# Performance work log

Measured on AMD Instinct MI355X. Metric: run time of the kernel, lower is better.

## Reference

```python
import jax, jax.numpy as jnp
import numpy as np

Q, N, C, H, W = 200, 25, 640, 5, 5
TEMPERATURE = 0.1
EPS = 1e-8  # torch F.cosine_similarity eps


def setup_inputs() -> dict:
    key = jax.random.key(0)
    k1, k2 = jax.random.split(key)
    feature_q = jax.random.normal(k1, (Q, N, C, H, W), dtype=jnp.float32)
    feature_s = jax.random.normal(k2, (Q, N, C, H, W), dtype=jnp.float32)
    return {"feature_q": feature_q, "feature_s": feature_s}


def reference(feature_q, feature_s):
    # Correlation volume: contract over channels c -> [Q, N, Hs, Ws, Hq, Wq]
    corr = jnp.einsum('qncij,qnckl->qnijkl', feature_s, feature_q)

    # Co-attention: mean-pool over the opposite spatial dims, softmax over last axis
    s_att = jax.nn.softmax(corr.mean(axis=(4, 5)), axis=-1)  # [Q, N, Hs, Ws]
    q_att = jax.nn.softmax(corr.mean(axis=(2, 3)), axis=-1)  # [Q, N, Hq, Wq]

    # Support aggregation (mode='support'):
    # torch broadcast [1,Q,N,1,H,W]*[1,Q,N,C,H,W] then mean(dim=1)
    # == mean over q of s_att[q,n,h,w] * feature_s[q,n,c,h,w] -> [1,N,C,H,W]
    attended_s = (s_att[:, :, None, :, :] * feature_s).mean(axis=0, keepdims=True)

    # Query aggregation (mode='query'):
    # torch broadcast [1,Q',N,1,H,W]*[Q,1,N,C,H,W] then mean(dim=1=Q')
    # == feature_q[q,n,c,h,w] * mean_{q'} q_att[q',n,h,w] -> [Q,N,C,H,W]
    # (fused form: avoids materializing the [Q,Q,N,C,H,W] intermediate)
    attended_q = feature_q * q_att.mean(axis=0)[None, :, None, :, :]

    # Cosine similarity along last dim (W), torch semantics with eps clamp
    dot = jnp.sum(attended_s * attended_q, axis=-1)               # [Q,N,C,H]
    norm_s = jnp.maximum(jnp.sqrt(jnp.sum(attended_s * attended_s, axis=-1)), EPS)
    norm_q = jnp.maximum(jnp.sqrt(jnp.sum(attended_q * attended_q, axis=-1)), EPS)
    similarity_score = dot / (norm_s * norm_q) / TEMPERATURE      # [Q,N,C,H]
    return similarity_score
```

## Files before the change

### kernel.cpp

```cpp
#include <hip/hip_runtime.h>

constexpr int Qn = 200;
constexpr int Nn = 25;
constexpr int Cn = 640;
constexpr int Hn = 5;
constexpr int Wn = 5;
constexpr int HWn = Hn * Wn;
constexpr int CHW = Cn * HWn;
constexpr float TEMP_INV = 10.0f;
constexpr float EPSC = 1e-8f;

typedef const float __attribute__((address_space(1)))* gbl_f;
typedef float __attribute__((address_space(3)))* lds_f;

__device__ __forceinline__ float wave_sum(float v) {
    v += __shfl_down(v, 32); v += __shfl_down(v, 16); v += __shfl_down(v, 8);
    v += __shfl_down(v, 4);  v += __shfl_down(v, 2);  v += __shfl_down(v, 1);
    return v;
}

__global__ __launch_bounds__(256) void attn_kernel(
    const float* __restrict__ fq, const float* __restrict__ fs,
    float* __restrict__ s_att, float* __restrict__ qbar)
{
    __shared__ float lds[4 * 3200];

    const int qn   = blockIdx.x;
    const int n    = qn % Nn;
    const int tid  = threadIdx.x;
    const int lane = tid & 63;
    const int wave = tid >> 6;

    const float* fq_t = fq + (size_t)qn * CHW;
    const float* fs_t = fs + (size_t)qn * CHW;
    float* ldsq = &lds[wave * 3200];
    float* ldss = ldsq + 1600;

    float ms[HWn], mq[HWn];
#pragma unroll
    for (int p = 0; p < HWn; ++p) { ms[p] = 0.f; mq[p] = 0.f; }

    for (int tile = wave; tile < 10; tile += 4) {
        const float* gq = fq_t + tile * 1600;
        const float* gs = fs_t + tile * 1600;

        asm volatile("s_waitcnt lgkmcnt(0)" ::: "memory");

#pragma unroll
        for (int i = 0; i < 6; ++i) {
            __builtin_amdgcn_global_load_lds((gbl_f)(gq + (i * 64 + lane) * 4),
                                             (lds_f)(ldsq + i * 256), 16, 0, 0);
            __builtin_amdgcn_global_load_lds((gbl_f)(gs + (i * 64 + lane) * 4),
                                             (lds_f)(ldss + i * 256), 16, 0, 0);
        }
        __builtin_amdgcn_global_load_lds((gbl_f)(gq + 1536 + lane),
                                         (lds_f)(ldsq + 1536), 4, 0, 0);
        __builtin_amdgcn_global_load_lds((gbl_f)(gs + 1536 + lane),
                                         (lds_f)(ldss + 1536), 4, 0, 0);
        asm volatile("s_waitcnt vmcnt(0)" ::: "memory");

        const float* rq = ldsq + lane * HWn;
        const float* rs = ldss + lane * HWn;
        float vq[HWn], vs[HWn];
        float sq = 0.f, ssv = 0.f;
#pragma unroll
        for (int p = 0; p < HWn; ++p) { vq[p] = rq[p]; sq += vq[p]; }
#pragma unroll
        for (int p = 0; p < HWn; ++p) { vs[p] = rs[p]; ssv += vs[p]; }
#pragma unroll
        for (int p = 0; p < HWn; ++p) {
            ms[p] += vs[p] * sq;
            mq[p] += vq[p] * ssv;
        }
    }

    __syncthreads();

    float* red = lds;
    float* fm  = lds + 200;
#pragma unroll
    for (int p = 0; p < HWn; ++p) {
        float v = wave_sum(ms[p]);
        if (lane == 0) red[wave * 50 + p] = v;
        float u = wave_sum(mq[p]);
        if (lane == 0) red[wave * 50 + HWn + p] = u;
    }
    __syncthreads();
    if (tid < 50) {
        fm[tid] = red[tid] + red[50 + tid] + red[100 + tid] + red[150 + tid];
    }
    __syncthreads();

    if (tid < 10) {
        const int r = tid;
        const float* row = (r < 5) ? &fm[r * 5] : &fm[HWn + (r - 5) * 5];
        float v[5];
        float mx = -1e30f;
#pragma unroll
        for (int j = 0; j < 5; ++j) {
            v[j] = row[j] * (1.0f / HWn);
            mx = fmaxf(mx, v[j]);
        }
        float s = 0.f;
#pragma unroll
        for (int j = 0; j < 5; ++j) { v[j] = __expf(v[j] - mx); s += v[j]; }
        const float inv = 1.0f / s;
        if (r < 5) {
#pragma unroll
            for (int j = 0; j < 5; ++j)
                s_att[(size_t)qn * HWn + r * 5 + j] = v[j] * inv;
        } else {
#pragma unroll
            for (int j = 0; j < 5; ++j)
                atomicAdd(&qbar[n * HWn + (r - 5) * 5 + j],
                          v[j] * inv * (1.0f / Qn));
        }
    }
}

__global__ __launch_bounds__(256) void agg_kernel(
    const float* __restrict__ fs, const float* __restrict__ s_att,
    float* __restrict__ att_s)
{
    constexpr int QCH = 40;
    __shared__ float w_lds[QCH * HWn];
    const int n  = blockIdx.y;
    const int q0 = blockIdx.z * QCH;

    for (int i = threadIdx.x; i < QCH * HWn; i += 256) {
        const int q = q0 + i / HWn;
        const int hw = i % HWn;
        w_lds[i] = s_att[(size_t)(q * Nn + n) * HWn + hw];
    }
    __syncthreads();

    const int f4 = blockIdx.x * 256 + threadIdx.x;
    if (f4 >= CHW / 4) return;
    const int f = f4 * 4;
    const int hw0 = f % HWn, hw1 = (f + 1) % HWn,
              hw2 = (f + 2) % HWn, hw3 = (f + 3) % HWn;

    float4 acc = make_float4(0.f, 0.f, 0.f, 0.f);
#pragma unroll 4
    for (int qi = 0; qi < QCH; ++qi) {
        const int q = q0 + qi;
        const float4 v = *(const float4*)(fs + (size_t)(q * Nn + n) * CHW + f);
        const float* w = &w_lds[qi * HWn];
        acc.x += w[hw0] * v.x;
        acc.y += w[hw1] * v.y;
        acc.z += w[hw2] * v.z;
        acc.w += w[hw3] * v.w;
    }
    float* dst = att_s + (size_t)n * CHW + f;
    atomicAdd(dst + 0, acc.x * (1.0f / Qn));
    atomicAdd(dst + 1, acc.y * (1.0f / Qn));
    atomicAdd(dst + 2, acc.z * (1.0f / Qn));
    atomicAdd(dst + 3, acc.w * (1.0f / Qn));
}

__global__ __launch_bounds__(256) void cos_kernel(
    const float* __restrict__ fq, const float* __restrict__ att_s,
    const float* __restrict__ qbar, float* __restrict__ out)
{
    const size_t idx = (size_t)blockIdx.x * 256 + threadIdx.x;
    if (idx >= (size_t)Qn * Nn * Cn * Hn) return;
    const int h = (int)(idx % Hn);
    const size_t t = idx / Hn;
    const int c = (int)(t % Cn);
    const size_t qn = t / Cn;
    const int n = (int)(qn % Nn);

    const float* fqr = fq + (qn * Cn + c) * HWn + h * Wn;
    const float* asr = att_s + ((size_t)n * Cn + c) * HWn + h * Wn;
    const float* qb  = qbar + n * HWn + h * Wn;

    float dot = 0.f, ns2 = 0.f, nq2 = 0.f;
#pragma unroll
    for (int w = 0; w < Wn; ++w) {
        const float aq = fqr[w] * qb[w];
        const float as = asr[w];
        dot += as * aq;
        ns2 += as * as;
        nq2 += aq * aq;
    }
    const float ns = fmaxf(sqrtf(ns2), EPSC);
    const float nq = fmaxf(sqrtf(nq2), EPSC);
    out[idx] = dot / (ns * nq) * TEMP_INV;
}

extern "C" void kernel_launch(void* const* d_in, const int* in_sizes, int n_in,
                              void* d_out, int out_size, void* d_ws, size_t ws_size,
                              hipStream_t stream)
{
    const float* fq = (const float*)d_in[0];
    const float* fs = (const float*)d_in[1];
    float* out = (float*)d_out;

    float* s_att = (float*)d_ws;
    float* qbar  = s_att + (size_t)Qn * Nn * HWn;
    float* att_s = qbar + 1024;

    hipMemsetAsync(qbar, 0, (1024 + (size_t)Nn * CHW) * sizeof(float), stream);

    attn_kernel<<<Qn * Nn, 256, 0, stream>>>(fq, fs, s_att, qbar);

    dim3 g2((CHW / 4 + 255) / 256, Nn, 5);
    agg_kernel<<<g2, 256, 0, stream>>>(fs, s_att, att_s);

    const size_t total = (size_t)Qn * Nn * Cn * Hn;
    cos_kernel<<<(unsigned)((total + 255) / 256), 256, 0, stream>>>(fq, att_s, qbar, out);
}
```

Baseline: 766.0 us.

## Use single-wave attention blocks with software-pipelined LDS staging

```diff
diff --git a/kernel.cpp b/kernel.cpp
--- a/kernel.cpp
+++ b/kernel.cpp
@@ -13,108 +13,111 @@
 typedef const float __attribute__((address_space(1)))* gbl_f;
 typedef float __attribute__((address_space(3)))* lds_f;
 
-__device__ __forceinline__ float wave_sum(float v) {
-    v += __shfl_down(v, 32); v += __shfl_down(v, 16); v += __shfl_down(v, 8);
-    v += __shfl_down(v, 4);  v += __shfl_down(v, 2);  v += __shfl_down(v, 1);
-    return v;
-}
-
-__global__ __launch_bounds__(256) void attn_kernel(
+__device__ __forceinline__ void stage_tile(const float* g, float* b, int lane) {
+#pragma unroll
+    for (int i = 0; i < 6; ++i)
+        __builtin_amdgcn_global_load_lds((gbl_f)(g + i * 256 + lane * 4),
+                                         (lds_f)(b + i * 256), 16, 0, 0);
+    __builtin_amdgcn_global_load_lds((gbl_f)(g + 1536 + lane),
+                                     (lds_f)(b + 1536), 4, 0, 0);
+}
+
+__global__ __launch_bounds__(64) void attn_kernel(
     const float* __restrict__ fq, const float* __restrict__ fs,
     float* __restrict__ s_att, float* __restrict__ qbar)
 {
-    __shared__ float lds[4 * 3200];
+    __shared__ float bq[1600];
+    __shared__ float bs[1600];
 
     const int qn   = blockIdx.x;
     const int n    = qn % Nn;
-    const int tid  = threadIdx.x;
-    const int lane = tid & 63;
-    const int wave = tid >> 6;
+    const int lane = threadIdx.x;
 
     const float* fq_t = fq + (size_t)qn * CHW;
     const float* fs_t = fs + (size_t)qn * CHW;
-    float* ldsq = &lds[wave * 3200];
-    float* ldss = ldsq + 1600;
+
+    stage_tile(fq_t, bq, lane);
+    stage_tile(fs_t, bs, lane);
 
     float ms[HWn], mq[HWn];
 #pragma unroll
     for (int p = 0; p < HWn; ++p) { ms[p] = 0.f; mq[p] = 0.f; }
 
-    for (int tile = wave; tile < 10; tile += 4) {
-        const float* gq = fq_t + tile * 1600;
-        const float* gs = fs_t + tile * 1600;
-
+    for (int t = 0; t < 10; ++t) {
+        asm volatile("s_waitcnt vmcnt(7)" ::: "memory");
+        float vq[HWn];
+        float sq = 0.f;
+        const float* rq = bq + lane * HWn;
+#pragma unroll
+        for (int p = 0; p < HWn; ++p) { vq[p] = rq[p]; sq += vq[p]; }
         asm volatile("s_waitcnt lgkmcnt(0)" ::: "memory");
-
-#pragma unroll
-        for (int i = 0; i < 6; ++i) {
-            __builtin_amdgcn_global_load_lds((gbl_f)(gq + (i * 64 + lane) * 4),
-                                             (lds_f)(ldsq + i * 256), 16, 0, 0);
-            __builtin_amdgcn_global_load_lds((gbl_f)(gs + (i * 64 + lane) * 4),
-                                             (lds_f)(ldss + i * 256), 16, 0, 0);
-        }
-        __builtin_amdgcn_global_load_lds((gbl_f)(gq + 1536 + lane),
-                                         (lds_f)(ldsq + 1536), 4, 0, 0);
-        __builtin_amdgcn_global_load_lds((gbl_f)(gs + 1536 + lane),
-                                         (lds_f)(ldss + 1536), 4, 0, 0);
-        asm volatile("s_waitcnt vmcnt(0)" ::: "memory");
-
-        const float* rq = ldsq + lane * HWn;
-        const float* rs = ldss + lane * HWn;
-        float vq[HWn], vs[HWn];
-        float sq = 0.f, ssv = 0.f;
-#pragma unroll
-        for (int p = 0; p < HWn; ++p) { vq[p] = rq[p]; sq += vq[p]; }
-#pragma unroll
-        for (int p = 0; p < HWn; ++p) { vs[p] = rs[p]; ssv += vs[p]; }
+        if (t < 9) stage_tile(fq_t + (t + 1) * 1600, bq, lane);
+
+        if (t < 9) asm volatile("s_waitcnt vmcnt(7)" ::: "memory");
+        else       asm volatile("s_waitcnt vmcnt(0)" ::: "memory");
+        float vs[HWn];
+        float ss = 0.f;
+        const float* rs = bs + lane * HWn;
+#pragma unroll
+        for (int p = 0; p < HWn; ++p) { vs[p] = rs[p]; ss += vs[p]; }
+        asm volatile("s_waitcnt lgkmcnt(0)" ::: "memory");
+        if (t < 9) stage_tile(fs_t + (t + 1) * 1600, bs, lane);
+
 #pragma unroll
         for (int p = 0; p < HWn; ++p) {
             ms[p] += vs[p] * sq;
-            mq[p] += vq[p] * ssv;
-        }
-    }
-
-    __syncthreads();
-
-    float* red = lds;
-    float* fm  = lds + 200;
+            mq[p] += vq[p] * ss;
+        }
+    }
+
 #pragma unroll
     for (int p = 0; p < HWn; ++p) {
-        float v = wave_sum(ms[p]);
-        if (lane == 0) red[wave * 50 + p] = v;
-        float u = wave_sum(mq[p]);
-        if (lane == 0) red[wave * 50 + HWn + p] = u;
-    }
-    __syncthreads();
-    if (tid < 50) {
-        fm[tid] = red[tid] + red[50 + tid] + red[100 + tid] + red[150 + tid];
-    }
-    __syncthreads();
-
-    if (tid < 10) {
-        const int r = tid;
-        const float* row = (r < 5) ? &fm[r * 5] : &fm[HWn + (r - 5) * 5];
-        float v[5];
-        float mx = -1e30f;
-#pragma unroll
-        for (int j = 0; j < 5; ++j) {
-            v[j] = row[j] * (1.0f / HWn);
-            mx = fmaxf(mx, v[j]);
-        }
-        float s = 0.f;
-#pragma unroll
-        for (int j = 0; j < 5; ++j) { v[j] = __expf(v[j] - mx); s += v[j]; }
-        const float inv = 1.0f / s;
-        if (r < 5) {
-#pragma unroll
-            for (int j = 0; j < 5; ++j)
-                s_att[(size_t)qn * HWn + r * 5 + j] = v[j] * inv;
-        } else {
-#pragma unroll
-            for (int j = 0; j < 5; ++j)
-                atomicAdd(&qbar[n * HWn + (r - 5) * 5 + j],
-                          v[j] * inv * (1.0f / Qn));
-        }
+        float a = ms[p], b = mq[p];
+#pragma unroll
+        for (int d = 1; d < 64; d <<= 1) {
+            a += __shfl_xor(a, d);
+            b += __shfl_xor(b, d);
+        }
+        ms[p] = a; mq[p] = b;
+    }
+
+    constexpr float inv25 = 1.0f / HWn;
+#pragma unroll
+    for (int r = 0; r < 5; ++r) {
+        {
+            float v[5];
+#pragma unroll
+            for (int j = 0; j < 5; ++j) v[j] = ms[r * 5 + j] * inv25;
+            float mx = fmaxf(fmaxf(fmaxf(v[0], v[1]), fmaxf(v[2], v[3])), v[4]);
+            float s = 0.f;
+#pragma unroll
+            for (int j = 0; j < 5; ++j) { v[j] = __expf(v[j] - mx); s += v[j]; }
+            const float inv = 1.0f / s;
+#pragma unroll
+            for (int j = 0; j < 5; ++j) ms[r * 5 + j] = v[j] * inv;
+        }
+        {
+            float v[5];
+#pragma unroll
+            for (int j = 0; j < 5; ++j) v[j] = mq[r * 5 + j] * inv25;
+            float mx = fmaxf(fmaxf(fmaxf(v[0], v[1]), fmaxf(v[2], v[3])), v[4]);
+            float s = 0.f;
+#pragma unroll
+            for (int j = 0; j < 5; ++j) { v[j] = __expf(v[j] - mx); s += v[j]; }
+            const float inv = (1.0f / s) * (1.0f / Qn);
+#pragma unroll
+            for (int j = 0; j < 5; ++j) mq[r * 5 + j] = v[j] * inv;
+        }
+    }
+
+    if (lane == 0) {
+        float* dst = s_att + (size_t)qn * HWn;
+#pragma unroll
+        for (int j = 0; j < HWn; ++j) dst[j] = ms[j];
+    } else if (lane == 32) {
+        float* dst = qbar + n * HWn;
+#pragma unroll
+        for (int j = 0; j < HWn; ++j) atomicAdd(dst + j, mq[j]);
     }
 }
 
@@ -202,7 +205,7 @@
 
     hipMemsetAsync(qbar, 0, (1024 + (size_t)Nn * CHW) * sizeof(float), stream);
 
-    attn_kernel<<<Qn * Nn, 256, 0, stream>>>(fq, fs, s_att, qbar);
+    attn_kernel<<<Qn * Nn, 64, 0, stream>>>(fq, fs, s_att, qbar);
 
     dim3 g2((CHW / 4 + 255) / 256, Nn, 5);
     agg_kernel<<<g2, 256, 0, stream>>>(fs, s_att, att_s);
```

Measured after the change: 770.9 us. About the same (+0.6%).

## Restructure attn kernel to block-cooperative tiles with split q/s thread roles

Applied to the files above, without the earlier changes.

```diff
diff --git a/kernel.cpp b/kernel.cpp
--- a/kernel.cpp
+++ b/kernel.cpp
@@ -10,20 +10,12 @@
 constexpr float TEMP_INV = 10.0f;
 constexpr float EPSC = 1e-8f;
 
-typedef const float __attribute__((address_space(1)))* gbl_f;
-typedef float __attribute__((address_space(3)))* lds_f;
-
-__device__ __forceinline__ float wave_sum(float v) {
-    v += __shfl_down(v, 32); v += __shfl_down(v, 16); v += __shfl_down(v, 8);
-    v += __shfl_down(v, 4);  v += __shfl_down(v, 2);  v += __shfl_down(v, 1);
-    return v;
-}
-
 __global__ __launch_bounds__(256) void attn_kernel(
     const float* __restrict__ fq, const float* __restrict__ fs,
     float* __restrict__ s_att, float* __restrict__ qbar)
 {
-    __shared__ float lds[4 * 3200];
+    __shared__ float buf[6400];
+    __shared__ float sums[256];
 
     const int qn   = blockIdx.x;
     const int n    = qn % Nn;
@@ -31,67 +23,68 @@
     const int lane = tid & 63;
     const int wave = tid >> 6;
 
-    const float* fq_t = fq + (size_t)qn * CHW;
-    const float* fs_t = fs + (size_t)qn * CHW;
-    float* ldsq = &lds[wave * 3200];
-    float* ldss = ldsq + 1600;
-
-    float ms[HWn], mq[HWn];
-#pragma unroll
-    for (int p = 0; p < HWn; ++p) { ms[p] = 0.f; mq[p] = 0.f; }
-
-    for (int tile = wave; tile < 10; tile += 4) {
-        const float* gq = fq_t + tile * 1600;
-        const float* gs = fs_t + tile * 1600;
-
-        asm volatile("s_waitcnt lgkmcnt(0)" ::: "memory");
-
-#pragma unroll
-        for (int i = 0; i < 6; ++i) {
-            __builtin_amdgcn_global_load_lds((gbl_f)(gq + (i * 64 + lane) * 4),
-                                             (lds_f)(ldsq + i * 256), 16, 0, 0);
-            __builtin_amdgcn_global_load_lds((gbl_f)(gs + (i * 64 + lane) * 4),
-                                             (lds_f)(ldss + i * 256), 16, 0, 0);
-        }
-        __builtin_amdgcn_global_load_lds((gbl_f)(gq + 1536 + lane),
-                                         (lds_f)(ldsq + 1536), 4, 0, 0);
-        __builtin_amdgcn_global_load_lds((gbl_f)(gs + 1536 + lane),
-                                         (lds_f)(ldss + 1536), 4, 0, 0);
-        asm volatile("s_waitcnt vmcnt(0)" ::: "memory");
-
-        const float* rq = ldsq + lane * HWn;
-        const float* rs = ldss + lane * HWn;
-        float vq[HWn], vs[HWn];
-        float sq = 0.f, ssv = 0.f;
-#pragma unroll
-        for (int p = 0; p < HWn; ++p) { vq[p] = rq[p]; sq += vq[p]; }
-#pragma unroll
-        for (int p = 0; p < HWn; ++p) { vs[p] = rs[p]; ssv += vs[p]; }
-#pragma unroll
-        for (int p = 0; p < HWn; ++p) {
-            ms[p] += vs[p] * sq;
-            mq[p] += vq[p] * ssv;
-        }
-    }
-
-    __syncthreads();
-
-    float* red = lds;
-    float* fm  = lds + 200;
+    const float4* fq4 = (const float4*)(fq + (size_t)qn * CHW);
+    const float4* fs4 = (const float4*)(fs + (size_t)qn * CHW);
+
+    const bool is_s = (tid >= 128);
+    const int rbase = is_s ? 3200 + (tid - 128) * HWn : tid * HWn;
+
+    float acc[HWn];
+#pragma unroll
+    for (int p = 0; p < HWn; ++p) acc[p] = 0.f;
+
+    for (int t = 0; t < 5; ++t) {
+        __syncthreads();
+        const int off = t * 800;
+#pragma unroll
+        for (int k = 0; k < 6; ++k) {
+            const int j = tid + k * 256;
+            const float4 v = (j < 800) ? fq4[off + j] : fs4[off + j - 800];
+            *(float4*)&buf[j * 4] = v;
+        }
+        if (tid < 64) {
+            const int j = tid + 1536;
+            *(float4*)&buf[j * 4] = fs4[off + j - 800];
+        }
+        __syncthreads();
+
+        const float* row = &buf[rbase];
+        float r[HWn];
+        float s = 0.f;
+#pragma unroll
+        for (int p = 0; p < HWn; ++p) { r[p] = row[p]; s += r[p]; }
+        sums[tid] = s;
+        __syncthreads();
+
+        const float ps = is_s ? sums[tid - 128] : sums[tid + 128];
+#pragma unroll
+        for (int p = 0; p < HWn; ++p) acc[p] += r[p] * ps;
+    }
+
+    __syncthreads();
+
 #pragma unroll
     for (int p = 0; p < HWn; ++p) {
-        float v = wave_sum(ms[p]);
-        if (lane == 0) red[wave * 50 + p] = v;
-        float u = wave_sum(mq[p]);
-        if (lane == 0) red[wave * 50 + HWn + p] = u;
+        float a = acc[p];
+#pragma unroll
+        for (int d = 1; d < 64; d <<= 1) a += __shfl_xor(a, d);
+        acc[p] = a;
+    }
+    if (lane == 0) {
+#pragma unroll
+        for (int p = 0; p < HWn; ++p) sums[wave * HWn + p] = acc[p];
     }
     __syncthreads();
     if (tid < 50) {
-        fm[tid] = red[tid] + red[50 + tid] + red[100 + tid] + red[150 + tid];
+        float v;
+        if (tid < 25) v = sums[50 + tid] + sums[75 + tid];
+        else          v = sums[tid - 25] + sums[tid];
+        sums[100 + tid] = v;
     }
     __syncthreads();
 
     if (tid < 10) {
+        const float* fm = &sums[100];
         const int r = tid;
         const float* row = (r < 5) ? &fm[r * 5] : &fm[HWn + (r - 5) * 5];
         float v[5];
```

Measured after the change: 757.7 us. Within noise of the previous version (-1.1%).
